# Performance work log

Hardware: AMD Instinct MI355X
Metric: run time of the kernel (lower is better)

Reference implementation:

```python
import jax, jax.numpy as jnp
import numpy as np

B = 2
C = 256          # hidden_dim / d_model
NH = 8           # attention heads
NL = 4           # feature levels
NP = 4           # sampling points per head per level
DH = C // NH
FF = 1024
NLAYERS = 6
SHAPES = [(64, 64), (32, 32), (16, 16), (8, 8)]
CIN = 256
OUT_CH = 2
IMG = 256


def setup_inputs() -> dict:
    key = jax.random.key(0)
    ks = iter(jax.random.split(key, 64))

    def nrm(shape, s=0.02):
        return jax.random.normal(next(ks), shape, jnp.float32) * s

    inp = {}
    for i, (h, w) in enumerate(SHAPES):
        inp[f"f{i}"] = jax.random.normal(next(ks), (B, CIN, h, w), jnp.float32)
    # input_proj: 1x1 conv + GroupNorm per level
    inp["proj_w"] = nrm((NL, C, CIN))
    inp["proj_b"] = jnp.zeros((NL, C), jnp.float32)
    inp["gn_w"] = jnp.ones((NL, C), jnp.float32)
    inp["gn_b"] = jnp.zeros((NL, C), jnp.float32)
    inp["level_embed"] = nrm((NL, C), 1.0)
    # 6 encoder layers (stacked params)
    inp["so_w"] = nrm((NLAYERS, NH * NL * NP * 2, C))   # sampling offsets
    inp["so_b"] = nrm((NLAYERS, NH * NL * NP * 2), 0.1)
    inp["aw_w"] = nrm((NLAYERS, NH * NL * NP, C))       # attention weights
    inp["aw_b"] = jnp.zeros((NLAYERS, NH * NL * NP), jnp.float32)
    inp["vp_w"] = nrm((NLAYERS, C, C))                   # value proj
    inp["vp_b"] = jnp.zeros((NLAYERS, C), jnp.float32)
    inp["op_w"] = nrm((NLAYERS, C, C))                   # output proj
    inp["op_b"] = jnp.zeros((NLAYERS, C), jnp.float32)
    inp["n1_w"] = jnp.ones((NLAYERS, C), jnp.float32)
    inp["n1_b"] = jnp.zeros((NLAYERS, C), jnp.float32)
    inp["l1_w"] = nrm((NLAYERS, FF, C))
    inp["l1_b"] = jnp.zeros((NLAYERS, FF), jnp.float32)
    inp["l2_w"] = nrm((NLAYERS, C, FF))
    inp["l2_b"] = jnp.zeros((NLAYERS, C), jnp.float32)
    inp["n2_w"] = jnp.ones((NLAYERS, C), jnp.float32)
    inp["n2_b"] = jnp.zeros((NLAYERS, C), jnp.float32)
    # classifier head convs
    inp["c1_w"] = nrm((64, C, 3, 3))
    inp["c1_b"] = jnp.zeros((64,), jnp.float32)
    inp["c2_w"] = nrm((OUT_CH, 64, 3, 3))
    inp["c2_b"] = jnp.zeros((OUT_CH,), jnp.float32)
    return inp


def group_norm(x, w, b, groups=32, eps=1e-5):
    Bq, Cc, H, W = x.shape
    xg = x.reshape(Bq, groups, Cc // groups, H, W)
    mu = xg.mean((2, 3, 4), keepdims=True)
    var = xg.var((2, 3, 4), keepdims=True)
    xg = (xg - mu) * jax.lax.rsqrt(var + eps)
    return xg.reshape(Bq, Cc, H, W) * w[None, :, None, None] + b[None, :, None, None]


def layer_norm(x, w, b, eps=1e-5):
    mu = x.mean(-1, keepdims=True)
    var = x.var(-1, keepdims=True)
    return (x - mu) * jax.lax.rsqrt(var + eps) * w + b


def pos_embed_sine(h, w, num_feats=C // 2):
    # PositionEmbeddingSine(normalize=True), mask all-False -> cumsum of ones
    eps = 1e-6
    scale = 2.0 * np.pi
    y = (jnp.arange(1, h + 1, dtype=jnp.float32) / (h + eps)) * scale
    x = (jnp.arange(1, w + 1, dtype=jnp.float32) / (w + eps)) * scale
    dim_t = 10000.0 ** (2.0 * (jnp.arange(num_feats) // 2).astype(jnp.float32) / num_feats)

    def enc(v):
        p = v[:, None] / dim_t  # [n, num_feats]
        return jnp.stack([jnp.sin(p[:, 0::2]), jnp.cos(p[:, 1::2])], -1).reshape(v.shape[0], num_feats)

    pe_y = enc(y)  # [h, 128]
    pe_x = enc(x)  # [w, 128]
    pos = jnp.concatenate([
        jnp.broadcast_to(pe_y[:, None, :], (h, w, num_feats)),
        jnp.broadcast_to(pe_x[None, :, :], (h, w, num_feats)),
    ], -1)  # [h, w, C], channels = (y, x)
    return pos.reshape(h * w, C)


def reference_points(shapes):
    pts = []
    for h, w in shapes:
        ry = (jnp.arange(h, dtype=jnp.float32) + 0.5) / h
        rx = (jnp.arange(w, dtype=jnp.float32) + 0.5) / w
        gy, gx = jnp.meshgrid(ry, rx, indexing='ij')
        pts.append(jnp.stack([gx, gy], -1).reshape(-1, 2))
    return jnp.concatenate(pts, 0)  # [Lq, 2] (x, y)


def bilinear_sample(v, x, y, Hl, Wl):
    # v: [B, NH, S, DH]; x, y: [B, Lq, NH, NP] pixel coords (align_corners=False, zero padding)
    x0 = jnp.floor(x); y0 = jnp.floor(y)
    fx = x - x0; fy = y - y0
    out = 0.0
    for dx, dy, wgt in ((0, 0, (1 - fx) * (1 - fy)), (1, 0, fx * (1 - fy)),
                        (0, 1, (1 - fx) * fy), (1, 1, fx * fy)):
        xi = x0 + dx; yi = y0 + dy
        valid = ((xi >= 0) & (xi < Wl) & (yi >= 0) & (yi < Hl)).astype(v.dtype)
        idx = (jnp.clip(yi, 0, Wl and Hl - 1) * Wl + jnp.clip(xi, 0, Wl - 1)).astype(jnp.int32)
        idx = (jnp.clip(yi, 0, Hl - 1) * Wl + jnp.clip(xi, 0, Wl - 1)).astype(jnp.int32)
        idxh = idx.transpose(0, 2, 1, 3).reshape(idx.shape[0], NH, -1)  # [B,NH,Lq*NP]
        g = jnp.take_along_axis(v, idxh[..., None], axis=2)             # [B,NH,Lq*NP,DH]
        w_ = (wgt * valid).transpose(0, 2, 1, 3).reshape(idx.shape[0], NH, -1, 1)
        out = out + g * w_
    return out  # [B, NH, Lq*NP, DH]


def ms_deform_attn(query, value_in, ref, starts,
                   so_w, so_b, aw_w, aw_b, vp_w, vp_b, op_w, op_b):
    Bq, Lq, _ = query.shape
    value = value_in @ vp_w.T + vp_b                                  # [B, Lin, C]
    value = value.reshape(Bq, -1, NH, DH).transpose(0, 2, 1, 3)       # [B, NH, Lin, DH]
    off = (query @ so_w.T + so_b).reshape(Bq, Lq, NH, NL, NP, 2)
    aw = (query @ aw_w.T + aw_b).reshape(Bq, Lq, NH, NL * NP)
    aw = jax.nn.softmax(aw, -1).reshape(Bq, Lq, NH, NL, NP)
    norm = jnp.array([[w, h] for (h, w) in SHAPES], jnp.float32)       # [NL, 2] (x, y)
    # sampling locations: ref (same across levels, valid_ratios=1) + normalized offsets
    loc = ref[None, :, None, None, None, :] + off / norm[None, None, None, :, None, :]
    out = jnp.zeros((Bq, NH, Lq, DH), jnp.float32)
    for l, (Hl, Wl) in enumerate(SHAPES):
        vl = jax.lax.dynamic_slice_in_dim(value, starts[l], Hl * Wl, axis=2)
        x = loc[:, :, :, l, :, 0] * Wl - 0.5
        y = loc[:, :, :, l, :, 1] * Hl - 0.5
        samp = bilinear_sample(vl, x, y, Hl, Wl).reshape(Bq, NH, Lq, NP, DH)
        out = out + jnp.einsum('bhqp,bhqpd->bhqd', aw[:, :, :, l].transpose(0, 2, 1, 3), samp)
    out = out.transpose(0, 2, 1, 3).reshape(Bq, Lq, C)
    return out @ op_w.T + op_b


def conv3x3(x, w, b):
    y = jax.lax.conv_general_dilated(x, w, (1, 1), ((1, 1), (1, 1)),
                                     dimension_numbers=('NCHW', 'OIHW', 'NCHW'))
    return y + b[None, :, None, None]


def reference(f0, f1, f2, f3, proj_w, proj_b, gn_w, gn_b, level_embed,
              so_w, so_b, aw_w, aw_b, vp_w, vp_b, op_w, op_b,
              n1_w, n1_b, l1_w, l1_b, l2_w, l2_b, n2_w, n2_b,
              c1_w, c1_b, c2_w, c2_b):
    feats = [f0, f1, f2, f3]
    srcs, poss = [], []
    for l, (h, w) in enumerate(SHAPES):
        x = jnp.einsum('oc,bchw->bohw', proj_w[l], feats[l]) + proj_b[l][None, :, None, None]
        x = group_norm(x, gn_w[l], gn_b[l])
        srcs.append(x.reshape(B, C, h * w).transpose(0, 2, 1))   # [B, HW, C]
        poss.append(pos_embed_sine(h, w) + level_embed[l])        # [HW, C]
    src = jnp.concatenate(srcs, 1)       # [B, Lq, C]
    pos = jnp.concatenate(poss, 0)       # [Lq, C]
    ref = reference_points(SHAPES)
    starts = np.cumsum([0] + [h * w for h, w in SHAPES])[:-1].tolist()
    x = src
    for i in range(NLAYERS):  # dropout=0 (eval mode)
        q = x + pos[None]
        a = ms_deform_attn(q, x, ref, starts,
                           so_w[i], so_b[i], aw_w[i], aw_b[i],
                           vp_w[i], vp_b[i], op_w[i], op_b[i])
        x = layer_norm(x + a, n1_w[i], n1_b[i])
        ff = jax.nn.relu(x @ l1_w[i].T + l1_b[i]) @ l2_w[i].T + l2_b[i]
        x = layer_norm(x + ff, n2_w[i], n2_b[i])
    h0, w0 = SHAPES[0]
    layer0 = x[:, :h0 * w0].reshape(B, h0, w0, C).transpose(0, 3, 1, 2)
    y = jax.nn.relu(conv3x3(layer0, c1_w, c1_b))
    y = conv3x3(y, c2_w, c2_b)
    return jax.image.resize(y, (B, OUT_CH, IMG, IMG), method='bilinear')
```

## Files before the change

### kernel.cpp

```cpp
#include <hip/hip_runtime.h>
#include <hip/hip_bf16.h>
#include <math.h>

#define LQ 5440
#define CDIM 256
#define BATCH 2
#define FFDIM 1024

typedef __attribute__((ext_vector_type(8))) short bf16x8;
typedef __attribute__((ext_vector_type(4))) float f32x4;

typedef __attribute__((address_space(1))) void* gas1_t;
typedef __attribute__((address_space(3))) void* las3_t;

__device__ __forceinline__ void async16(const void* g, void* l) {
  __builtin_amdgcn_global_load_lds((gas1_t)g, (las3_t)l, 16, 0, 0);
}

#define WAIT_VM5() asm volatile("s_waitcnt vmcnt(5)" ::: "memory")
#define WAIT_VM4() asm volatile("s_waitcnt vmcnt(4)" ::: "memory")
#define WAIT_VM3() asm volatile("s_waitcnt vmcnt(3)" ::: "memory")
#define WAIT_VM2() asm volatile("s_waitcnt vmcnt(2)" ::: "memory")
#define WAIT_VM0() asm volatile("s_waitcnt vmcnt(0)" ::: "memory")

__device__ __forceinline__ void get_chunk(int chunk, int& l, int& row0) {
  if (chunk < 64)      { l = 0; row0 = chunk * 64; }
  else if (chunk < 80) { l = 1; row0 = (chunk - 64) * 64; }
  else if (chunk < 84) { l = 2; row0 = (chunk - 80) * 64; }
  else                 { l = 3; row0 = 0; }
}

template <bool RELU, bool OUT_F32, bool OUT_B16, bool REMAP>
__global__ __launch_bounds__(256, 2) void gemm_bf16_kernel(
    const __hip_bfloat16* __restrict__ A, const __hip_bfloat16* __restrict__ Wt,
    const float* __restrict__ bias, float* __restrict__ C,
    __hip_bfloat16* __restrict__ Cb, int M, int N, int K,
    int mrows, long obase, long obstride) {
  __shared__ __hip_bfloat16 As[3][128 * 32];
  __shared__ __hip_bfloat16 Bs[3][128 * 32];
  const int tid = threadIdx.x;
  const int bm = blockIdx.y * 128, bn = blockIdx.x * 128;
  const int lane = tid & 63, wave = tid >> 6;
  const int wr = wave >> 1, wc = wave & 1;
  const int srow = tid >> 2;
  const int scol = (tid & 3) * 8;
  const int lo0 = srow * 32 + scol;
  const int lo1 = (64 + srow) * 32 + scol;
  const __hip_bfloat16* ga0 = A + (size_t)(bm + srow) * K + scol;
  const __hip_bfloat16* ga1 = A + (size_t)(bm + 64 + srow) * K + scol;
  const __hip_bfloat16* gb0 = Wt + (size_t)(bn + srow) * K + scol;
  const __hip_bfloat16* gb1 = Wt + (size_t)(bn + 64 + srow) * K + scol;

  const int nt = K >> 5;
  async16(ga0, &As[0][lo0]);
  async16(ga1, &As[0][lo1]);
  async16(gb0, &Bs[0][lo0]);
  async16(gb1, &Bs[0][lo1]);
  async16(ga0 + 32, &As[1][lo0]);
  async16(ga1 + 32, &As[1][lo1]);
  async16(gb0 + 32, &Bs[1][lo0]);
  async16(gb1 + 32, &Bs[1][lo1]);

  f32x4 acc[4][4] = {};
  const int fr = lane & 15;
  const int ksub = (lane >> 4) * 8;

  int cur = 0, nxt = 2;
  for (int t = 0; t < nt; ++t) {
    if (t == nt - 1) WAIT_VM0(); else WAIT_VM4();
    __builtin_amdgcn_s_barrier();
    asm volatile("" ::: "memory");
    bf16x8 af[4], bfv[4];
    const __hip_bfloat16* as = As[cur];
    const __hip_bfloat16* bs = Bs[cur];
#pragma unroll
    for (int mi = 0; mi < 4; ++mi)
      af[mi] = *(const bf16x8*)&as[(wr * 64 + mi * 16 + fr) * 32 + ksub];
#pragma unroll
    for (int nj = 0; nj < 4; ++nj)
      bfv[nj] = *(const bf16x8*)&bs[(wc * 64 + nj * 16 + fr) * 32 + ksub];
    if (t + 2 < nt) {
      const int ko = (t + 2) * 32;
      async16(ga0 + ko, &As[nxt][lo0]);
      async16(ga1 + ko, &As[nxt][lo1]);
      async16(gb0 + ko, &Bs[nxt][lo0]);
      async16(gb1 + ko, &Bs[nxt][lo1]);
    }
#pragma unroll
    for (int mi = 0; mi < 4; ++mi)
#pragma unroll
      for (int nj = 0; nj < 4; ++nj)
        acc[mi][nj] = __builtin_amdgcn_mfma_f32_16x16x32_bf16(af[mi], bfv[nj],
                                                              acc[mi][nj], 0, 0, 0);
    cur = (cur == 2) ? 0 : cur + 1;
    nxt = (nxt == 2) ? 0 : nxt + 1;
  }

  const int cc = lane & 15;
  const int rbase = (lane >> 4) * 4;
  float bcol[4];
#pragma unroll
  for (int nj = 0; nj < 4; ++nj) bcol[nj] = bias[bn + wc * 64 + nj * 16 + cc];
#pragma unroll
  for (int mi = 0; mi < 4; ++mi)
#pragma unroll
    for (int nj = 0; nj < 4; ++nj) {
      int col = bn + wc * 64 + nj * 16 + cc;
#pragma unroll
      for (int r = 0; r < 4; ++r) {
        int row = bm + wr * 64 + mi * 16 + rbase + r;
        float v = acc[mi][nj][r] + bcol[nj];
        if (RELU) v = fmaxf(v, 0.f);
        if (OUT_F32) {
          size_t oaddr;
          if (REMAP)
            oaddr = (size_t)obase +
                    (row < mrows ? (size_t)row * N
                                 : (size_t)obstride + (size_t)(row - mrows) * N) +
                    col;
          else
            oaddr = (size_t)row * N + col;
          C[oaddr] = v;
        }
        if (OUT_B16) Cb[(size_t)row * N + col] = __float2bfloat16(v);
      }
    }
}

template <bool OUT_F32, bool OUT_B16>
__device__ __forceinline__ void gemm64_body(
    const __hip_bfloat16* __restrict__ A, const __hip_bfloat16* __restrict__ Wt,
    const float* __restrict__ bias, float* __restrict__ C,
    __hip_bfloat16* __restrict__ Cb, int bm, int bn, int N, int K,
    __hip_bfloat16 (*As)[64 * 32], __hip_bfloat16 (*Bs)[128 * 32]) {
  const int tid = threadIdx.x;
  const int lane = tid & 63, wv = tid >> 6;
  const int srow = tid >> 2, scol = (tid & 3) * 8;
  const int loA = srow * 32 + scol;
  const int loB1 = (64 + srow) * 32 + scol;
  const __hip_bfloat16* ga = A + (size_t)(bm + srow) * K + scol;
  const __hip_bfloat16* gb0 = Wt + (size_t)(bn + srow) * K + scol;
  const __hip_bfloat16* gb1 = Wt + (size_t)(bn + 64 + srow) * K + scol;
  const int nt = K >> 5;
  async16(ga, &As[0][loA]);
  async16(gb0, &Bs[0][loA]);
  async16(gb1, &Bs[0][loB1]);
  async16(ga + 32, &As[1][loA]);
  async16(gb0 + 32, &Bs[1][loA]);
  async16(gb1 + 32, &Bs[1][loB1]);

  f32x4 acc[4][2] = {};
  const int fr = lane & 15, ksub = (lane >> 4) * 8;
  int cur = 0, nxt = 2;
  for (int t = 0; t < nt; ++t) {
    if (t == nt - 1) WAIT_VM0(); else WAIT_VM3();
    __builtin_amdgcn_s_barrier();
    asm volatile("" ::: "memory");
    bf16x8 af[4], bfv[2];
#pragma unroll
    for (int mi = 0; mi < 4; ++mi)
      af[mi] = *(const bf16x8*)&As[cur][(mi * 16 + fr) * 32 + ksub];
#pragma unroll
    for (int nj = 0; nj < 2; ++nj)
      bfv[nj] = *(const bf16x8*)&Bs[cur][(wv * 32 + nj * 16 + fr) * 32 + ksub];
    if (t + 2 < nt) {
      const int ko = (t + 2) * 32;
      async16(ga + ko, &As[nxt][loA]);
      async16(gb0 + ko, &Bs[nxt][loA]);
      async16(gb1 + ko, &Bs[nxt][loB1]);
    }
#pragma unroll
    for (int mi = 0; mi < 4; ++mi)
#pragma unroll
      for (int nj = 0; nj < 2; ++nj)
        acc[mi][nj] = __builtin_amdgcn_mfma_f32_16x16x32_bf16(af[mi], bfv[nj],
                                                              acc[mi][nj], 0, 0, 0);
    cur = (cur == 2) ? 0 : cur + 1;
    nxt = (nxt == 2) ? 0 : nxt + 1;
  }
  const int cc = lane & 15;
  const int rbase = (lane >> 4) * 4;
#pragma unroll
  for (int nj = 0; nj < 2; ++nj) {
    int col = bn + wv * 32 + nj * 16 + cc;
    float bb = bias[col];
#pragma unroll
    for (int mi = 0; mi < 4; ++mi)
#pragma unroll
      for (int r = 0; r < 4; ++r) {
        int row = bm + mi * 16 + rbase + r;
        float v = acc[mi][nj][r] + bb;
        if (OUT_F32) C[(size_t)row * N + col] = v;
        if (OUT_B16) Cb[(size_t)row * N + col] = __float2bfloat16(v);
      }
  }
}

__global__ __launch_bounds__(256, 4) void gemm_dual_kernel(
    const __hip_bfloat16* __restrict__ xb, const __hip_bfloat16* __restrict__ vw,
    const float* __restrict__ vb, __hip_bfloat16* __restrict__ valb,
    const __hip_bfloat16* __restrict__ qb, const __hip_bfloat16* __restrict__ sowa,
    const float* __restrict__ sbias, float* __restrict__ comb) {
  __shared__ __hip_bfloat16 As[3][64 * 32];
  __shared__ __hip_bfloat16 Bs[3][128 * 32];
  if (blockIdx.x < 340) {
    int i = blockIdx.x;
    gemm64_body<false, true>(xb, vw, vb, nullptr, valb, (i >> 1) * 64,
                             (i & 1) * 128, 256, 256, As, Bs);
  } else {
    int j = blockIdx.x - 340;
    gemm64_body<true, false>(qb, sowa, sbias, comb, nullptr, (j / 3) * 64,
                             (j % 3) * 128, 384, 256, As, Bs);
  }
}

template <bool EMIT_Q>
__global__ __launch_bounds__(256, 2) void gemm_ln_kernel(
    const __hip_bfloat16* __restrict__ A, const __hip_bfloat16* __restrict__ Wt,
    const float* __restrict__ bias, float* __restrict__ x,
    __hip_bfloat16* __restrict__ xb, __hip_bfloat16* __restrict__ qb,
    const float* __restrict__ pos, const float* __restrict__ lnw,
    const float* __restrict__ lnb, int K) {
  __shared__ __hip_bfloat16 As[3][32 * 32];
  __shared__ __hip_bfloat16 Bs[3][256 * 32];
  __shared__ float sred[4][32], ssred[4][32];
  const int tid = threadIdx.x;
  const int bm = blockIdx.x * 32;
  const int lane = tid & 63, wv = tid >> 6;
  const int srow = tid >> 2;
  const int arow = srow & 31;
  const int scol = (tid & 3) * 8;
  const int loA = arow * 32 + scol;
  const __hip_bfloat16* ga = A + (size_t)(bm + arow) * K + scol;
  const __hip_bfloat16* gb = Wt + (size_t)srow * K + scol;

  const int nt = K >> 5;
  auto stage = [&](int t, int buf) {
    const int ko = t * 32;
    async16(ga + ko, &As[buf][loA]);
#pragma unroll
    for (int i = 0; i < 4; ++i)
      async16(gb + (size_t)(64 * i) * K + ko, &Bs[buf][(64 * i + srow) * 32 + scol]);
  };
  stage(0, 0);
  stage(1, 1);

  f32x4 acc[2][4] = {};
  const int fr = lane & 15;
  const int ksub = (lane >> 4) * 8;

  int cur = 0, nxt = 2;
  for (int t = 0; t < nt; ++t) {
    if (t == nt - 1) WAIT_VM0(); else WAIT_VM5();
    __builtin_amdgcn_s_barrier();
    asm volatile("" ::: "memory");
    bf16x8 af[2], bfv[4];
#pragma unroll
    for (int mi = 0; mi < 2; ++mi)
      af[mi] = *(const bf16x8*)&As[cur][(mi * 16 + fr) * 32 + ksub];
#pragma unroll
    for (int nj = 0; nj < 4; ++nj)
      bfv[nj] = *(const bf16x8*)&Bs[cur][(wv * 64 + nj * 16 + fr) * 32 + ksub];
    if (t + 2 < nt) stage(t + 2, nxt);
#pragma unroll
    for (int mi = 0; mi < 2; ++mi)
#pragma unroll
      for (int nj = 0; nj < 4; ++nj)
        acc[mi][nj] = __builtin_amdgcn_mfma_f32_16x16x32_bf16(af[mi], bfv[nj],
                                                              acc[mi][nj], 0, 0, 0);
    cur = (cur == 2) ? 0 : cur + 1;
    nxt = (nxt == 2) ? 0 : nxt + 1;
  }

  const int cc = lane & 15;
  const int rbase = (lane >> 4) * 4;
  float bcol[4], wcol[4], bncol[4];
#pragma unroll
  for (int nj = 0; nj < 4; ++nj) {
    int col = wv * 64 + nj * 16 + cc;
    bcol[nj] = bias[col];
    wcol[nj] = lnw[col];
    bncol[nj] = lnb[col];
  }
#pragma unroll
  for (int mi = 0; mi < 2; ++mi)
#pragma unroll
    for (int r = 0; r < 4; ++r) {
      int grow = bm + mi * 16 + rbase + r;
#pragma unroll
      for (int nj = 0; nj < 4; ++nj) {
        int col = wv * 64 + nj * 16 + cc;
        acc[mi][nj][r] += bcol[nj] + x[(size_t)grow * 256 + col];
      }
    }
#pragma unroll
  for (int mi = 0; mi < 2; ++mi)
#pragma unroll
    for (int r = 0; r < 4; ++r) {
      float s = 0.f, ssq = 0.f;
#pragma unroll
      for (int nj = 0; nj < 4; ++nj) {
        float v = acc[mi][nj][r];
        s += v;
        ssq += v * v;
      }
#pragma unroll
      for (int m = 1; m < 16; m <<= 1) {
        s += __shfl_xor(s, m);
        ssq += __shfl_xor(ssq, m);
      }
      if (cc == 0) {
        int row = mi * 16 + rbase + r;
        sred[wv][row] = s;
        ssred[wv][row] = ssq;
      }
    }
  __syncthreads();
#pragma unroll
  for (int mi = 0; mi < 2; ++mi)
#pragma unroll
    for (int r = 0; r < 4; ++r) {
      int row = mi * 16 + rbase + r;
      int grow = bm + row;
      float s = sred[0][row] + sred[1][row] + sred[2][row] + sred[3][row];
      float ssq = ssred[0][row] + ssred[1][row] + ssred[2][row] + ssred[3][row];
      float mu = s * (1.0f / 256.0f);
      float var = ssq * (1.0f / 256.0f) - mu * mu;
      float rsig = rsqrtf(var + 1e-5f);
      int tokp = grow >= LQ ? grow - LQ : grow;
#pragma unroll
      for (int nj = 0; nj < 4; ++nj) {
        int col = wv * 64 + nj * 16 + cc;
        float xn = (acc[mi][nj][r] - mu) * rsig * wcol[nj] + bncol[nj];
        x[(size_t)grow * 256 + col] = xn;
        xb[(size_t)grow * 256 + col] = __float2bfloat16(xn);
        if (EMIT_Q)
          qb[(size_t)grow * 256 + col] =
              __float2bfloat16(xn + pos[(size_t)tokp * 256 + col]);
      }
    }
}

__global__ __launch_bounds__(256, 4) void conv1_mfma_kernel(
    const __hip_bfloat16* __restrict__ xb, const __hip_bfloat16* __restrict__ wc1,
    const float* __restrict__ bias, const __hip_bfloat16* __restrict__ zerob,
    __hip_bfloat16* __restrict__ c1o) {
  __shared__ __hip_bfloat16 As[3][64 * 32];
  __shared__ __hip_bfloat16 Bs[3][64 * 32];
  const int tid = threadIdx.x;
  const int b = blockIdx.x >> 6;
  const int pm = (blockIdx.x & 63) * 64;
  const int lane = tid & 63, wave = tid >> 6;
  const int sr = tid >> 2;
  const int sc = (tid & 3) * 8;
  const int lo = sr * 32 + sc;
  f32x4 acc[4] = {};
  const int fr = lane & 15, ksub = (lane >> 4) * 8;

  auto stage = [&](int kt, int buf) {
    int tap = kt >> 3;
    int kk = (kt & 7) * 32;
    int dy = tap / 3 - 1, dx = tap % 3 - 1;
    int hw = pm + sr;
    int y = (hw >> 6) + dy, x = (hw & 63) + dx;
    bool ok = (y >= 0 && y < 64 && x >= 0 && x < 64);
    const __hip_bfloat16* s =
        xb + ((size_t)(b * LQ) + y * 64 + x) * 256 + kk + sc;
    const __hip_bfloat16* wsrc = wc1 + (size_t)sr * 2304 + tap * 256 + kk + sc;
    async16(ok ? s : zerob, &As[buf][lo]);
    async16(wsrc, &Bs[buf][lo]);
  };
  stage(0, 0);
  stage(1, 1);
  int cur = 0, nxt = 2;
  for (int kt = 0; kt < 72; ++kt) {
    if (kt == 71) WAIT_VM0(); else WAIT_VM2();
    __builtin_amdgcn_s_barrier();
    asm volatile("" ::: "memory");
    bf16x8 af;
    bf16x8 bfv[4];
    af = *(const bf16x8*)&As[cur][(wave * 16 + fr) * 32 + ksub];
#pragma unroll
    for (int nj = 0; nj < 4; ++nj)
      bfv[nj] = *(const bf16x8*)&Bs[cur][(nj * 16 + fr) * 32 + ksub];
    if (kt + 2 < 72) stage(kt + 2, nxt);
#pragma unroll
    for (int nj = 0; nj < 4; ++nj)
      acc[nj] = __builtin_amdgcn_mfma_f32_16x16x32_bf16(af, bfv[nj], acc[nj], 0, 0, 0);
    cur = (cur == 2) ? 0 : cur + 1;
    nxt = (nxt == 2) ? 0 : nxt + 1;
  }
  const int cc = lane & 15;
  const int rbase = (lane >> 4) * 4;
#pragma unroll
  for (int nj = 0; nj < 4; ++nj) {
    int col = nj * 16 + cc;
    float bb = bias[col];
#pragma unroll
    for (int r = 0; r < 4; ++r) {
      int row = wave * 16 + rbase + r;
      float v = fmaxf(acc[nj][r] + bb, 0.f);
      c1o[(size_t)(b * 4096 + pm + row) * 64 + col] = __float2bfloat16(v);
    }
  }
}

__global__ void f2b_multi_kernel(const float* __restrict__ p0, const float* __restrict__ p1,
                                 const float* __restrict__ p2, const float* __restrict__ p3,
                                 const float* __restrict__ p4,
                                 __hip_bfloat16* __restrict__ o0, __hip_bfloat16* __restrict__ o1,
                                 __hip_bfloat16* __restrict__ o2, __hip_bfloat16* __restrict__ o3,
                                 __hip_bfloat16* __restrict__ o4) {
  int i = blockIdx.x * 256 + threadIdx.x;
  if (i >= 1048576) return;
  const float* in;
  __hip_bfloat16* out;
  int j;
  if (i < 65536)       { in = p0; out = o0; j = i; }
  else if (i < 163840) { in = p1; out = o1; j = i - 65536; }
  else if (i < 262144) { in = p2; out = o2; j = i - 163840; }
  else if (i < 655360) { in = p3; out = o3; j = i - 262144; }
  else                 { in = p4; out = o4; j = i - 655360; }
  float4 v = ((const float4*)in)[j];
  union { ushort4 u; __hip_bfloat16 h[4]; } p;
  p.h[0] = __float2bfloat16(v.x);
  p.h[1] = __float2bfloat16(v.y);
  p.h[2] = __float2bfloat16(v.z);
  p.h[3] = __float2bfloat16(v.w);
  ((ushort4*)out)[j] = p.u;
}

__global__ void sowa_prep_kernel(const float* __restrict__ so_w,
                                 const float* __restrict__ aw_w,
                                 const float* __restrict__ so_b,
                                 const float* __restrict__ aw_b,
                                 __hip_bfloat16* __restrict__ out,
                                 float* __restrict__ bias_out) {
  int i = blockIdx.x * 256 + threadIdx.x;
  if (i < 6 * 384 * 256) {
    int il = i / (384 * 256);
    int rem = i - il * 384 * 256;
    int n = rem >> 8, k = rem & 255;
    float v = (n < 256) ? so_w[(size_t)il * 65536 + n * 256 + k]
                        : aw_w[(size_t)il * 32768 + (n - 256) * 256 + k];
    out[i] = __float2bfloat16(v);
  } else if (i < 6 * 384 * 256 + 6 * 384) {
    int j = i - 6 * 384 * 256;
    int il = j / 384, n = j % 384;
    bias_out[j] = (n < 256) ? so_b[il * 256 + n] : aw_b[il * 128 + n - 256];
  }
}

__global__ void wc1_prep_kernel(const float* __restrict__ w,
                                __hip_bfloat16* __restrict__ out) {
  int i = blockIdx.x * 256 + threadIdx.x;
  if (i >= 64 * 2304) return;
  int oc = i / 2304, r = i % 2304;
  int tap = r >> 8, ic = r & 255;
  out[i] = __float2bfloat16(w[(size_t)oc * 2304 + ic * 9 + tap]);
}

__global__ __launch_bounds__(256) void transpose_f_kernel(
    const float* __restrict__ f0, const float* __restrict__ f1,
    const float* __restrict__ f2, const float* __restrict__ f3,
    __hip_bfloat16* __restrict__ ft) {
  __shared__ float tile[64][65];
  const int HWs[4] = {4096, 1024, 256, 64};
  const int STs[4] = {0, 4096, 5120, 5376};
  int chunk = blockIdx.x, c0 = blockIdx.y * 64, b = blockIdx.z;
  int l, row0;
  get_chunk(chunk, l, row0);
  const float* fin = (l == 0) ? f0 : (l == 1) ? f1 : (l == 2) ? f2 : f3;
  const int HW = HWs[l];
  int t = threadIdx.x;
  int cr = t >> 4, hc4 = (t & 15) * 4;
#pragma unroll
  for (int p = 0; p < 4; ++p) {
    int c = c0 + p * 16 + cr;
    float4 v = *(const float4*)&fin[(size_t)(b * 256 + c) * HW + row0 + hc4];
    tile[p * 16 + cr][hc4 + 0] = v.x;
    tile[p * 16 + cr][hc4 + 1] = v.y;
    tile[p * 16 + cr][hc4 + 2] = v.z;
    tile[p * 16 + cr][hc4 + 3] = v.w;
  }
  __syncthreads();
  size_t obase = (size_t)2 * STs[l] * 256 + ((size_t)b * HW + row0) * 256 + c0;
#pragma unroll
  for (int p = 0; p < 4; ++p) {
    int r = p * 16 + cr;
    union { ushort4 u; __hip_bfloat16 h[4]; } pk;
    pk.h[0] = __float2bfloat16(tile[hc4 + 0][r]);
    pk.h[1] = __float2bfloat16(tile[hc4 + 1][r]);
    pk.h[2] = __float2bfloat16(tile[hc4 + 2][r]);
    pk.h[3] = __float2bfloat16(tile[hc4 + 3][r]);
    *(ushort4*)&ft[obase + (size_t)r * 256 + hc4] = pk.u;
  }
}

__global__ __launch_bounds__(256) void gn_part_kernel(const float* __restrict__ x,
                                                      float2* __restrict__ part) {
  const int STs[4] = {0, 4096, 5120, 5376};
  int chunk = blockIdx.x, b = blockIdx.y;
  int l, row0;
  get_chunk(chunk, l, row0);
  size_t base = ((size_t)b * LQ + STs[l] + row0) * 256;
  int t = threadIdx.x;
  int col4 = t & 63, rb = t >> 6;
  float s = 0.f, ss = 0.f;
#pragma unroll 4
  for (int i = 0; i < 16; ++i) {
    int r = rb + i * 4;
    float4 v = *(const float4*)&x[base + (size_t)r * 256 + col4 * 4];
    s += v.x + v.y + v.z + v.w;
    ss += v.x * v.x + v.y * v.y + v.z * v.z + v.w * v.w;
  }
  __shared__ float sA[256], sB[256];
  sA[t] = s;
  sB[t] = ss;
  __syncthreads();
  if (t < 64) {
    s = sA[t] + sA[t + 64] + sA[t + 128] + sA[t + 192];
    ss = sB[t] + sB[t + 64] + sB[t + 128] + sB[t + 192];
    sA[t] = s;
    sB[t] = ss;
  }
  __syncthreads();
  if (t < 32)
    part[((size_t)b * 85 + chunk) * 32 + t] =
        make_float2(sA[2 * t] + sA[2 * t + 1], sB[2 * t] + sB[2 * t + 1]);
}

__global__ void gn_finalize_kernel(const float2* __restrict__ part,
                                   float2* __restrict__ stats) {
  int t = threadIdx.x;
  int b = t >> 7, rem = t & 127, l = rem >> 5, g = rem & 31;
  const int cnt_[4] = {64, 16, 4, 1};
  const int cb_[4] = {0, 64, 80, 84};
  const int HWs[4] = {4096, 1024, 256, 64};
  float s = 0.f, ss = 0.f;
  for (int i = 0; i < cnt_[l]; ++i) {
    float2 v = part[((size_t)b * 85 + cb_[l] + i) * 32 + g];
    s += v.x;
    ss += v.y;
  }
  float n = (float)(HWs[l] * 8);
  float mu = s / n;
  float var = ss / n - mu * mu;
  stats[(b * 4 + l) * 32 + g] = make_float2(mu, rsqrtf(var + 1e-5f));
}

__device__ __forceinline__ void get_level(int t, int& l, int& hw, int& Hl, int& Wl) {
  if (t < 4096)      { l = 0; hw = t;        Hl = 64; Wl = 64; }
  else if (t < 5120) { l = 1; hw = t - 4096; Hl = 32; Wl = 32; }
  else if (t < 5376) { l = 2; hw = t - 5120; Hl = 16; Wl = 16; }
  else               { l = 3; hw = t - 5376; Hl = 8;  Wl = 8;  }
}

__global__ void gn_apply_kernel(float* __restrict__ x, __hip_bfloat16* __restrict__ xb,
                                __hip_bfloat16* __restrict__ qb,
                                const float* __restrict__ pos,
                                const float2* __restrict__ stats,
                                const float* __restrict__ gw, const float* __restrict__ gb) {
  int idx = blockIdx.x * 256 + threadIdx.x;
  if (idx >= BATCH * LQ * CDIM) return;
  int c = idx & 255;
  int tok = idx >> 8;
  int b = tok / LQ, t = tok % LQ;
  int l, hw, Hl, Wl;
  get_level(t, l, hw, Hl, Wl);
  float2 st = stats[(b * 4 + l) * 32 + (c >> 3)];
  float v = (x[idx] - st.x) * st.y * gw[l * CDIM + c] + gb[l * CDIM + c];
  x[idx] = v;
  xb[idx] = __float2bfloat16(v);
  qb[idx] = __float2bfloat16(v + pos[t * 256 + c]);
}

__global__ void pos_embed_kernel(const float* __restrict__ level_embed,
                                 float* __restrict__ pos) {
  int idx = blockIdx.x * 256 + threadIdx.x;
  if (idx >= LQ * CDIM) return;
  int t = idx >> 8, c = idx & 255;
  int l, hw, Hl, Wl;
  get_level(t, l, hw, Hl, Wl);
  int y = hw / Wl, xx = hw % Wl;
  const float twopi = 6.28318530717958647692f;
  float v; int cc;
  if (c < 128) { v = (float)(y + 1) * twopi / ((float)Hl + 1e-6f); cc = c; }
  else         { v = (float)(xx + 1) * twopi / ((float)Wl + 1e-6f); cc = c - 128; }
  int k = cc >> 1;
  float dim_t = expf((float)k * (logf(10000.0f) / 64.0f));
  float p = v / dim_t;
  float e = (cc & 1) ? cosf(p) : sinf(p);
  pos[idx] = e + level_embed[l * CDIM + c];
}

__global__ void ref_kernel(float* __restrict__ ref) {
  int t = blockIdx.x * 256 + threadIdx.x;
  if (t >= LQ) return;
  int l, hw, Hl, Wl;
  get_level(t, l, hw, Hl, Wl);
  int y = hw / Wl, xx = hw % Wl;
  ref[t * 2]     = ((float)xx + 0.5f) / (float)Wl;
  ref[t * 2 + 1] = ((float)y + 0.5f) / (float)Hl;
}

__global__ __launch_bounds__(256) void deform_attn_kernel(
    const __hip_bfloat16* __restrict__ value, const float* __restrict__ comb,
    const float* __restrict__ ref, __hip_bfloat16* __restrict__ out) {
  const int Wl_[4] = {64, 32, 16, 8};
  const int st_[4] = {0, 4096, 5120, 5376};
  int gid = blockIdx.x * 64 + (threadIdx.x >> 2);
  int lane4 = threadIdx.x & 3;
  int h = gid & 7;
  int tok = gid >> 3;
  int b = tok / LQ;
  int qi = tok - b * LQ;

  const float4* awv = (const float4*)(comb + (size_t)tok * 384 + 256 + h * 16);
  float4 q0 = awv[0], q1 = awv[1], q2 = awv[2], q3 = awv[3];
  float logit[16] = {q0.x, q0.y, q0.z, q0.w, q1.x, q1.y, q1.z, q1.w,
                     q2.x, q2.y, q2.z, q2.w, q3.x, q3.y, q3.z, q3.w};
  float mx = -1e30f;
#pragma unroll
  for (int i = 0; i < 16; ++i) mx = fmaxf(mx, logit[i]);
  const float LOG2E = 1.4426950408889634f;
  float ssum = 0.f;
#pragma unroll
  for (int i = 0; i < 16; ++i) {
    logit[i] = exp2f((logit[i] - mx) * LOG2E);
    ssum += logit[i];
  }
  float inv = 1.0f / ssum;

  float rx = ref[qi * 2], ry = ref[qi * 2 + 1];
  const float4* offv = (const float4*)(comb + (size_t)tok * 384 + h * 32);
  float acc[8] = {};

#pragma unroll
  for (int l = 0; l < 4; ++l) {
    const int Wl = Wl_[l];
    const float fW = (float)Wl;
    const __hip_bfloat16* vbase =
        value + ((size_t)b * LQ + st_[l]) * CDIM + h * 32 + lane4 * 8;
    float bx = fmaf(rx, fW, -0.5f);
    float by = fmaf(ry, fW, -0.5f);
    float4 oa = offv[l * 2], ob = offv[l * 2 + 1];
    float oxs[4] = {oa.x, oa.z, ob.x, ob.z};
    float oys[4] = {oa.y, oa.w, ob.y, ob.w};
#pragma unroll
    for (int p = 0; p < 4; ++p) {
      float px = bx + oxs[p], py = by + oys[p];
      float wgt = logit[l * 4 + p] * inv;
      float fpx = floorf(px), fpy = floorf(py);
      int x0 = (int)fpx, y0 = (int)fpy;
      float fx = px - fpx, fy = py - fpy;
      float wx0 = (x0 >= 0 && x0 < Wl) ? (1.f - fx) : 0.f;
      float wx1 = (x0 >= -1 && x0 < Wl - 1) ? fx : 0.f;
      float wy0 = (y0 >= 0 && y0 < Wl) ? (wgt * (1.f - fy)) : 0.f;
      float wy1 = (y0 >= -1 && y0 < Wl - 1) ? (wgt * fy) : 0.f;
      int xc0 = min(max(x0, 0), Wl - 1);
      int xc1 = min(max(x0 + 1, 0), Wl - 1);
      int yc0 = min(max(y0, 0), Wl - 1);
      int yc1 = min(max(y0 + 1, 0), Wl - 1);
      const __hip_bfloat16* r0 = vbase + (size_t)(yc0 * Wl) * CDIM;
      const __hip_bfloat16* r1 = vbase + (size_t)(yc1 * Wl) * CDIM;
      bf16x8 u00 = *(const bf16x8*)(r0 + (size_t)xc0 * CDIM);
      bf16x8 u01 = *(const bf16x8*)(r0 + (size_t)xc1 * CDIM);
      bf16x8 u10 = *(const bf16x8*)(r1 + (size_t)xc0 * CDIM);
      bf16x8 u11 = *(const bf16x8*)(r1 + (size_t)xc1 * CDIM);
      float w00 = wy0 * wx0, w01 = wy0 * wx1, w10 = wy1 * wx0, w11 = wy1 * wx1;
#pragma unroll
      for (int k = 0; k < 8; ++k) {
        float v00 = __uint_as_float((unsigned)(unsigned short)u00[k] << 16);
        float v01 = __uint_as_float((unsigned)(unsigned short)u01[k] << 16);
        float v10 = __uint_as_float((unsigned)(unsigned short)u10[k] << 16);
        float v11 = __uint_as_float((unsigned)(unsigned short)u11[k] << 16);
        acc[k] = fmaf(w00, v00, acc[k]);
        acc[k] = fmaf(w01, v01, acc[k]);
        acc[k] = fmaf(w10, v10, acc[k]);
        acc[k] = fmaf(w11, v11, acc[k]);
      }
    }
  }
  union { bf16x8 u; __hip_bfloat16 hh[8]; } pk;
#pragma unroll
  for (int k = 0; k < 8; ++k) pk.hh[k] = __float2bfloat16(acc[k]);
  *(bf16x8*)(out + (size_t)tok * CDIM + h * 32 + lane4 * 8) = pk.u;
}

__global__ __launch_bounds__(256) void conv2_part_kernel(
    const __hip_bfloat16* __restrict__ c1o, const float* __restrict__ w,
    float* __restrict__ part) {
  int pix = blockIdx.x * 256 + threadIdx.x;
  int tap = blockIdx.y, b = blockIdx.z;
  int y = pix >> 6, x = pix & 63;
  int dy = tap / 3 - 1, dx = tap % 3 - 1;
  int yy = y + dy, xx = x + dx;
  bool ok = (yy >= 0 && yy < 64 && xx >= 0 && xx < 64);
  float a0 = 0.f, a1 = 0.f;
  if (ok) {
    const __hip_bfloat16* row = c1o + (size_t)(b * 4096 + yy * 64 + xx) * 64;
#pragma unroll
    for (int ic4 = 0; ic4 < 16; ++ic4) {
      ushort4 u = *(const ushort4*)(row + ic4 * 4);
      float f0 = __uint_as_float((unsigned)u.x << 16);
      float f1 = __uint_as_float((unsigned)u.y << 16);
      float f2 = __uint_as_float((unsigned)u.z << 16);
      float f3 = __uint_as_float((unsigned)u.w << 16);
      int ic = ic4 * 4;
      a0 = fmaf(w[(ic + 0) * 9 + tap], f0, a0);
      a0 = fmaf(w[(ic + 1) * 9 + tap], f1, a0);
      a0 = fmaf(w[(ic + 2) * 9 + tap], f2, a0);
      a0 = fmaf(w[(ic + 3) * 9 + tap], f3, a0);
      a1 = fmaf(w[576 + (ic + 0) * 9 + tap], f0, a1);
      a1 = fmaf(w[576 + (ic + 1) * 9 + tap], f1, a1);
      a1 = fmaf(w[576 + (ic + 2) * 9 + tap], f2, a1);
      a1 = fmaf(w[576 + (ic + 3) * 9 + tap], f3, a1);
    }
  }
  float2 o = make_float2(a0, a1);
  *(float2*)&part[((size_t)(tap * BATCH + b) * 4096 + pix) * 2] = o;
}

__global__ void conv2_reduce_kernel(const float* __restrict__ part,
                                    const float* __restrict__ bias,
                                    float* __restrict__ out) {
  int i = blockIdx.x * 256 + threadIdx.x;
  if (i >= BATCH * 4096) return;
  int b = i >> 12, pix = i & 4095;
  float s0 = bias[0], s1 = bias[1];
#pragma unroll
  for (int tap = 0; tap < 9; ++tap) {
    float2 v = *(const float2*)&part[((size_t)(tap * BATCH + b) * 4096 + pix) * 2];
    s0 += v.x; s1 += v.y;
  }
  *(float2*)&out[(size_t)i * 2] = make_float2(s0, s1);
}

__global__ void upsample_kernel(const float* __restrict__ in, float* __restrict__ out) {
  int idx = blockIdx.x * 256 + threadIdx.x;
  if (idx >= BATCH * 2 * 256 * 256) return;
  int X = idx & 255, Y = (idx >> 8) & 255, p = idx >> 16;
  int b = p >> 1, oc = p & 1;
  float tx = ((float)X + 0.5f) * 0.25f - 0.5f;
  float ty = ((float)Y + 0.5f) * 0.25f - 0.5f;
  float fxf = floorf(tx), fyf = floorf(ty);
  int x0 = (int)fxf, y0 = (int)fyf;
  float fx = tx - fxf, fy = ty - fyf;
  int x0c = min(max(x0, 0), 63), x1c = min(max(x0 + 1, 0), 63);
  int y0c = min(max(y0, 0), 63), y1c = min(max(y0 + 1, 0), 63);
  const float* ip = in + (size_t)b * 4096 * 2 + oc;
  float v = (1.f - fy) * ((1.f - fx) * ip[(y0c * 64 + x0c) * 2] + fx * ip[(y0c * 64 + x1c) * 2]) +
            fy * ((1.f - fx) * ip[(y1c * 64 + x0c) * 2] + fx * ip[(y1c * 64 + x1c) * 2]);
  out[idx] = v;
}

extern "C" void kernel_launch(void* const* d_in, const int* in_sizes, int n_in,
                              void* d_out, int out_size, void* d_ws, size_t ws_size,
                              hipStream_t stream) {
  const float* f[4] = {(const float*)d_in[0], (const float*)d_in[1],
                       (const float*)d_in[2], (const float*)d_in[3]};
  const float* proj_w = (const float*)d_in[4];
  const float* proj_b = (const float*)d_in[5];
  const float* gn_w = (const float*)d_in[6];
  const float* gn_b = (const float*)d_in[7];
  const float* level_embed = (const float*)d_in[8];
  const float* so_w = (const float*)d_in[9];
  const float* so_b = (const float*)d_in[10];
  const float* aw_w = (const float*)d_in[11];
  const float* aw_b = (const float*)d_in[12];
  const float* vp_w = (const float*)d_in[13];
  const float* vp_b = (const float*)d_in[14];
  const float* op_w = (const float*)d_in[15];
  const float* op_b = (const float*)d_in[16];
  const float* n1_w = (const float*)d_in[17];
  const float* n1_b = (const float*)d_in[18];
  const float* l1_w = (const float*)d_in[19];
  const float* l1_b = (const float*)d_in[20];
  const float* l2_w = (const float*)d_in[21];
  const float* l2_b = (const float*)d_in[22];
  const float* n2_w = (const float*)d_in[23];
  const float* n2_b = (const float*)d_in[24];
  const float* c1_w = (const float*)d_in[25];
  const float* c1_b = (const float*)d_in[26];
  const float* c2_w = (const float*)d_in[27];
  const float* c2_b = (const float*)d_in[28];
  (void)in_sizes; (void)n_in; (void)out_size; (void)ws_size;

  float* ws = (float*)d_ws;
  const size_t TOK = (size_t)BATCH * LQ * CDIM;
  size_t o = 0;
  float* x = ws + o;     o += TOK;
  float* comb = ws + o;  o += (size_t)BATCH * LQ * 384;
  float* pos = ws + o;   o += (size_t)LQ * CDIM;
  float* refb = ws + o;  o += 11008;
  float2* stats = (float2*)(ws + o); o += 512;
  float* zerof = ws + o; o += 256;
  float* sowa_bias = ws + o; o += 2304;
  float2* gnpart = (float2*)(ws + o); o += 11008;
  __hip_bfloat16* xb = (__hip_bfloat16*)(ws + o);    o += TOK / 2;
  __hip_bfloat16* qb = (__hip_bfloat16*)(ws + o);    o += TOK / 2;
  __hip_bfloat16* valb = (__hip_bfloat16*)(ws + o);  o += TOK / 2;
  __hip_bfloat16* attnb = (__hip_bfloat16*)(ws + o); o += TOK / 2;
  __hip_bfloat16* ftb = (__hip_bfloat16*)(ws + o);   o += TOK / 2;
  __hip_bfloat16* ff1b = (__hip_bfloat16*)(ws + o);  o += (size_t)BATCH * LQ * FFDIM / 2;
  __hip_bfloat16* sowa_wb = (__hip_bfloat16*)(ws + o); o += 294912;
  __hip_bfloat16* vp_wb = (__hip_bfloat16*)(ws + o); o += 196608;
  __hip_bfloat16* op_wb = (__hip_bfloat16*)(ws + o); o += 196608;
  __hip_bfloat16* l1_wb = (__hip_bfloat16*)(ws + o); o += 786432;
  __hip_bfloat16* l2_wb = (__hip_bfloat16*)(ws + o); o += 786432;
  __hip_bfloat16* proj_wb = (__hip_bfloat16*)(ws + o); o += 131072;
  __hip_bfloat16* wc1b = (__hip_bfloat16*)(ws + o);  o += 73728;
  __hip_bfloat16* c1ob = ff1b;
  float* part2 = (float*)(ff1b + 524288);
  float* c2o = part2 + 147456;

  const int HWs[4] = {4096, 1024, 256, 64};
  const int STs[4] = {0, 4096, 5120, 5376};

  hipMemsetAsync(zerof, 0, 1024, stream);
  sowa_prep_kernel<<<(6 * 384 * 256 + 6 * 384 + 255) / 256, 256, 0, stream>>>(
      so_w, aw_w, so_b, aw_b, sowa_wb, sowa_bias);
  wc1_prep_kernel<<<(147456 + 255) / 256, 256, 0, stream>>>(c1_w, wc1b);
  f2b_multi_kernel<<<(1048576 + 255) / 256, 256, 0, stream>>>(
      proj_w, vp_w, op_w, l1_w, l2_w, proj_wb, vp_wb, op_wb, l1_wb, l2_wb);

  transpose_f_kernel<<<dim3(85, 4, BATCH), 256, 0, stream>>>(f[0], f[1], f[2], f[3],
                                                             ftb);
  for (int l = 0; l < 4; ++l) {
    int M2 = 2 * HWs[l];
    gemm_bf16_kernel<false, true, false, true><<<dim3(2, M2 / 128), 256, 0, stream>>>(
        ftb + (size_t)2 * STs[l] * 256, proj_wb + (size_t)l * 65536,
        proj_b + (size_t)l * 256, x, nullptr, M2, 256, 256,
        HWs[l], (long)STs[l] * 256, (long)LQ * 256);
  }
  pos_embed_kernel<<<(LQ * CDIM + 255) / 256, 256, 0, stream>>>(level_embed, pos);
  ref_kernel<<<(LQ + 255) / 256, 256, 0, stream>>>(refb);
  gn_part_kernel<<<dim3(85, BATCH), 256, 0, stream>>>(x, gnpart);
  gn_finalize_kernel<<<1, 256, 0, stream>>>(gnpart, stats);
  {
    int n = BATCH * LQ * CDIM;
    gn_apply_kernel<<<(n + 255) / 256, 256, 0, stream>>>(x, xb, qb, pos, stats,
                                                         gn_w, gn_b);
  }

  const int M = BATCH * LQ;
  for (int i = 0; i < 6; ++i) {
    const __hip_bfloat16* sowa = sowa_wb + (size_t)i * 98304;
    const __hip_bfloat16* vw = vp_wb + (size_t)i * 65536;
    const __hip_bfloat16* ow = op_wb + (size_t)i * 65536;
    const __hip_bfloat16* w1 = l1_wb + (size_t)i * 262144;
    const __hip_bfloat16* w2 = l2_wb + (size_t)i * 262144;
    const float* vb = vp_b + (size_t)i * CDIM;
    const float* ob = op_b + (size_t)i * CDIM;
    const float* b1 = l1_b + (size_t)i * FFDIM;
    const float* b2 = l2_b + (size_t)i * CDIM;

    gemm_dual_kernel<<<850, 256, 0, stream>>>(xb, vw, vb, valb, qb, sowa,
                                              sowa_bias + i * 384, comb);
    deform_attn_kernel<<<BATCH * LQ * 8 / 64, 256, 0, stream>>>(valb, comb, refb,
                                                                attnb);
    gemm_ln_kernel<false><<<340, 256, 0, stream>>>(
        attnb, ow, ob, x, xb, nullptr, nullptr,
        n1_w + (size_t)i * CDIM, n1_b + (size_t)i * CDIM, CDIM);
    gemm_bf16_kernel<true, false, true, false><<<dim3(8, 85), 256, 0, stream>>>(
        xb, w1, b1, nullptr, ff1b, M, FFDIM, CDIM, 0, 0, 0);
    gemm_ln_kernel<true><<<340, 256, 0, stream>>>(
        ff1b, w2, b2, x, xb, qb, pos,
        n2_w + (size_t)i * CDIM, n2_b + (size_t)i * CDIM, FFDIM);
  }

  conv1_mfma_kernel<<<128, 256, 0, stream>>>(xb, wc1b, c1_b,
                                             (const __hip_bfloat16*)zerof, c1ob);
  conv2_part_kernel<<<dim3(16, 9, BATCH), 256, 0, stream>>>(c1ob, c2_w, part2);
  conv2_reduce_kernel<<<(BATCH * 4096 + 255) / 256, 256, 0, stream>>>(part2, c2_b,
                                                                      c2o);
  {
    int n = BATCH * 2 * 256 * 256;
    upsample_kernel<<<(n + 255) / 256, 256, 0, stream>>>(c2o, (float*)d_out);
  }
}
```

Baseline: 636.8 us.

## Merge input-proj launches, fuse pos/ref kernels, use 64-row tiles for FFN1

```diff
diff --git a/kernel.cpp b/kernel.cpp
--- a/kernel.cpp
+++ b/kernel.cpp
@@ -30,16 +30,28 @@
   else                 { l = 3; row0 = 0; }
 }
 
-template <bool RELU, bool OUT_F32, bool OUT_B16, bool REMAP>
-__global__ __launch_bounds__(256, 2) void gemm_bf16_kernel(
-    const __hip_bfloat16* __restrict__ A, const __hip_bfloat16* __restrict__ Wt,
-    const float* __restrict__ bias, float* __restrict__ C,
-    __hip_bfloat16* __restrict__ Cb, int M, int N, int K,
-    int mrows, long obase, long obstride) {
+__global__ __launch_bounds__(256, 2) void input_proj_kernel(
+    const __hip_bfloat16* __restrict__ ftb, const __hip_bfloat16* __restrict__ proj_wb,
+    const float* __restrict__ proj_b, float* __restrict__ x) {
+  const int HWs[4] = {4096, 1024, 256, 64};
+  const int STs[4] = {0, 4096, 5120, 5376};
+  int i = blockIdx.x, l, j;
+  if (i < 128)      { l = 0; j = i; }
+  else if (i < 160) { l = 1; j = i - 128; }
+  else if (i < 168) { l = 2; j = i - 160; }
+  else              { l = 3; j = i - 168; }
+  const int bm = (j >> 1) * 128, bn = (j & 1) * 128;
+  const int mrows = HWs[l];
+  const long obase = (long)STs[l] * 256;
+  const long obstride = (long)LQ * 256;
+  const __hip_bfloat16* A = ftb + (size_t)2 * STs[l] * 256;
+  const __hip_bfloat16* Wt = proj_wb + (size_t)l * 65536;
+  const float* bias = proj_b + l * 256;
+  const int K = 256, N = 256;
+
   __shared__ __hip_bfloat16 As[3][128 * 32];
   __shared__ __hip_bfloat16 Bs[3][128 * 32];
   const int tid = threadIdx.x;
-  const int bm = blockIdx.y * 128, bn = blockIdx.x * 128;
   const int lane = tid & 63, wave = tid >> 6;
   const int wr = wave >> 1, wc = wave & 1;
   const int srow = tid >> 2;
@@ -64,21 +76,18 @@
   f32x4 acc[4][4] = {};
   const int fr = lane & 15;
   const int ksub = (lane >> 4) * 8;
-
   int cur = 0, nxt = 2;
   for (int t = 0; t < nt; ++t) {
     if (t == nt - 1) WAIT_VM0(); else WAIT_VM4();
     __builtin_amdgcn_s_barrier();
     asm volatile("" ::: "memory");
     bf16x8 af[4], bfv[4];
-    const __hip_bfloat16* as = As[cur];
-    const __hip_bfloat16* bs = Bs[cur];
 #pragma unroll
     for (int mi = 0; mi < 4; ++mi)
-      af[mi] = *(const bf16x8*)&as[(wr * 64 + mi * 16 + fr) * 32 + ksub];
+      af[mi] = *(const bf16x8*)&As[cur][(wr * 64 + mi * 16 + fr) * 32 + ksub];
 #pragma unroll
     for (int nj = 0; nj < 4; ++nj)
-      bfv[nj] = *(const bf16x8*)&bs[(wc * 64 + nj * 16 + fr) * 32 + ksub];
+      bfv[nj] = *(const bf16x8*)&Bs[cur][(wc * 64 + nj * 16 + fr) * 32 + ksub];
     if (t + 2 < nt) {
       const int ko = (t + 2) * 32;
       async16(ga0 + ko, &As[nxt][lo0]);
@@ -109,25 +118,16 @@
 #pragma unroll
       for (int r = 0; r < 4; ++r) {
         int row = bm + wr * 64 + mi * 16 + rbase + r;
-        float v = acc[mi][nj][r] + bcol[nj];
-        if (RELU) v = fmaxf(v, 0.f);
-        if (OUT_F32) {
-          size_t oaddr;
-          if (REMAP)
-            oaddr = (size_t)obase +
-                    (row < mrows ? (size_t)row * N
-                                 : (size_t)obstride + (size_t)(row - mrows) * N) +
-                    col;
-          else
-            oaddr = (size_t)row * N + col;
-          C[oaddr] = v;
-        }
-        if (OUT_B16) Cb[(size_t)row * N + col] = __float2bfloat16(v);
+        size_t oaddr = (size_t)obase +
+                       (row < mrows ? (size_t)row * N
+                                    : (size_t)obstride + (size_t)(row - mrows) * N) +
+                       col;
+        x[oaddr] = acc[mi][nj][r] + bcol[nj];
       }
     }
 }
 
-template <bool OUT_F32, bool OUT_B16>
+template <bool RELU, bool OUT_F32, bool OUT_B16>
 __device__ __forceinline__ void gemm64_body(
     const __hip_bfloat16* __restrict__ A, const __hip_bfloat16* __restrict__ Wt,
     const float* __restrict__ bias, float* __restrict__ C,
@@ -190,6 +190,7 @@
       for (int r = 0; r < 4; ++r) {
         int row = bm + mi * 16 + rbase + r;
         float v = acc[mi][nj][r] + bb;
+        if (RELU) v = fmaxf(v, 0.f);
         if (OUT_F32) C[(size_t)row * N + col] = v;
         if (OUT_B16) Cb[(size_t)row * N + col] = __float2bfloat16(v);
       }
@@ -205,13 +206,23 @@
   __shared__ __hip_bfloat16 Bs[3][128 * 32];
   if (blockIdx.x < 340) {
     int i = blockIdx.x;
-    gemm64_body<false, true>(xb, vw, vb, nullptr, valb, (i >> 1) * 64,
-                             (i & 1) * 128, 256, 256, As, Bs);
+    gemm64_body<false, false, true>(xb, vw, vb, nullptr, valb, (i >> 1) * 64,
+                                    (i & 1) * 128, 256, 256, As, Bs);
   } else {
     int j = blockIdx.x - 340;
-    gemm64_body<true, false>(qb, sowa, sbias, comb, nullptr, (j / 3) * 64,
-                             (j % 3) * 128, 384, 256, As, Bs);
-  }
+    gemm64_body<false, true, false>(qb, sowa, sbias, comb, nullptr, (j / 3) * 64,
+                                    (j % 3) * 128, 384, 256, As, Bs);
+  }
+}
+
+__global__ __launch_bounds__(256, 4) void ffn1_kernel(
+    const __hip_bfloat16* __restrict__ xb, const __hip_bfloat16* __restrict__ w1,
+    const float* __restrict__ b1, __hip_bfloat16* __restrict__ ff1b) {
+  __shared__ __hip_bfloat16 As[3][64 * 32];
+  __shared__ __hip_bfloat16 Bs[3][128 * 32];
+  int i = blockIdx.x;
+  gemm64_body<true, false, true>(xb, w1, b1, nullptr, ff1b, (i >> 3) * 64,
+                                 (i & 7) * 128, 1024, 256, As, Bs);
 }
 
 template <bool EMIT_Q>
@@ -575,8 +586,8 @@
   qb[idx] = __float2bfloat16(v + pos[t * 256 + c]);
 }
 
-__global__ void pos_embed_kernel(const float* __restrict__ level_embed,
-                                 float* __restrict__ pos) {
+__global__ void pos_ref_kernel(const float* __restrict__ level_embed,
+                               float* __restrict__ pos, float* __restrict__ ref) {
   int idx = blockIdx.x * 256 + threadIdx.x;
   if (idx >= LQ * CDIM) return;
   int t = idx >> 8, c = idx & 255;
@@ -592,16 +603,10 @@
   float p = v / dim_t;
   float e = (cc & 1) ? cosf(p) : sinf(p);
   pos[idx] = e + level_embed[l * CDIM + c];
-}
-
-__global__ void ref_kernel(float* __restrict__ ref) {
-  int t = blockIdx.x * 256 + threadIdx.x;
-  if (t >= LQ) return;
-  int l, hw, Hl, Wl;
-  get_level(t, l, hw, Hl, Wl);
-  int y = hw / Wl, xx = hw % Wl;
-  ref[t * 2]     = ((float)xx + 0.5f) / (float)Wl;
-  ref[t * 2 + 1] = ((float)y + 0.5f) / (float)Hl;
+  if (c == 0) {
+    ref[t * 2]     = ((float)xx + 0.5f) / (float)Wl;
+    ref[t * 2 + 1] = ((float)y + 0.5f) / (float)Hl;
+  }
 }
 
 __global__ __launch_bounds__(256) void deform_attn_kernel(
@@ -815,9 +820,6 @@
   float* part2 = (float*)(ff1b + 524288);
   float* c2o = part2 + 147456;
 
-  const int HWs[4] = {4096, 1024, 256, 64};
-  const int STs[4] = {0, 4096, 5120, 5376};
-
   hipMemsetAsync(zerof, 0, 1024, stream);
   sowa_prep_kernel<<<(6 * 384 * 256 + 6 * 384 + 255) / 256, 256, 0, stream>>>(
       so_w, aw_w, so_b, aw_b, sowa_wb, sowa_bias);
@@ -827,15 +829,8 @@
 
   transpose_f_kernel<<<dim3(85, 4, BATCH), 256, 0, stream>>>(f[0], f[1], f[2], f[3],
                                                              ftb);
-  for (int l = 0; l < 4; ++l) {
-    int M2 = 2 * HWs[l];
-    gemm_bf16_kernel<false, true, false, true><<<dim3(2, M2 / 128), 256, 0, stream>>>(
-        ftb + (size_t)2 * STs[l] * 256, proj_wb + (size_t)l * 65536,
-        proj_b + (size_t)l * 256, x, nullptr, M2, 256, 256,
-        HWs[l], (long)STs[l] * 256, (long)LQ * 256);
-  }
-  pos_embed_kernel<<<(LQ * CDIM + 255) / 256, 256, 0, stream>>>(level_embed, pos);
-  ref_kernel<<<(LQ + 255) / 256, 256, 0, stream>>>(refb);
+  input_proj_kernel<<<170, 256, 0, stream>>>(ftb, proj_wb, proj_b, x);
+  pos_ref_kernel<<<(LQ * CDIM + 255) / 256, 256, 0, stream>>>(level_embed, pos, refb);
   gn_part_kernel<<<dim3(85, BATCH), 256, 0, stream>>>(x, gnpart);
   gn_finalize_kernel<<<1, 256, 0, stream>>>(gnpart, stats);
   {
@@ -844,7 +839,6 @@
                                                          gn_w, gn_b);
   }
 
-  const int M = BATCH * LQ;
   for (int i = 0; i < 6; ++i) {
     const __hip_bfloat16* sowa = sowa_wb + (size_t)i * 98304;
     const __hip_bfloat16* vw = vp_wb + (size_t)i * 65536;
@@ -863,8 +857,7 @@
     gemm_ln_kernel<false><<<340, 256, 0, stream>>>(
         attnb, ow, ob, x, xb, nullptr, nullptr,
         n1_w + (size_t)i * CDIM, n1_b + (size_t)i * CDIM, CDIM);
-    gemm_bf16_kernel<true, false, true, false><<<dim3(8, 85), 256, 0, stream>>>(
-        xb, w1, b1, nullptr, ff1b, M, FFDIM, CDIM, 0, 0, 0);
+    ffn1_kernel<<<1360, 256, 0, stream>>>(xb, w1, b1, ff1b);
     gemm_ln_kernel<true><<<340, 256, 0, stream>>>(
         ff1b, w2, b2, x, xb, qb, pos,
         n2_w + (size_t)i * CDIM, n2_b + (size_t)i * CDIM, FFDIM);
```

After: 621.0 us. 1.03x faster.
